# Optimization experiments

Hardware: AMD Instinct MI355X
Metric: run time of the kernel (lower is better)

## Reference

```python
import jax, jax.numpy as jnp
import numpy as np

B, S, SEG, D = 2, 128, 128, 768
RL, H, DK = 16, 8, 64
DV = D // H            # 96, dim_value = dim // heads
NRPF = D // H          # num_rel_pos_features
N = S * RL             # 2048 attention tokens
SCALE = DK ** -0.5


def setup_inputs() -> dict:
    key = jax.random.key(0)
    ks = jax.random.split(key, 12)
    g = lambda k, sh: jax.random.normal(k, sh, jnp.float32) * 0.02
    return {
        'x': jax.random.normal(ks[0], (B, S, SEG, D), jnp.float32),
        'ln_g': jnp.ones((D,), jnp.float32),
        'ln_b': jnp.zeros((D,), jnp.float32),
        'Wq': g(ks[1], (D, H * DK)),
        'Wk': g(ks[2], (D, H * DK)),
        'Wv': g(ks[3], (D, H * DV)),
        'Wr': g(ks[4], (NRPF, H * DK)),
        'r_w_bias': g(ks[5], (H, DK)),
        'r_r_bias': g(ks[6], (H, DK)),
        'Wo': g(ks[7], (H * DV, D)),
        'bo': jnp.zeros((D,), jnp.float32),
        'pos_emb': g(ks[8], (2 * N - 1, NRPF)),  # relative position features, dist -(N-1)..(N-1)
    }


def _layernorm(x, g, b, eps=1e-5):
    mu = jnp.mean(x, -1, keepdims=True)
    var = jnp.var(x, -1, keepdims=True)
    return (x - mu) * jax.lax.rsqrt(var + eps) * g + b


def _relative_shift(t):
    # t: [b, h, n, 2n-1] -> [b, h, n, n] (enformer-style shift)
    b, h, n, _ = t.shape
    t = jnp.pad(t, ((0, 0), (0, 0), (0, 0), (1, 0)))      # [b,h,n,2n]
    t = t.reshape(b, h, 2 * n, n)[:, :, 1:, :]            # [b,h,2n-1,n]
    t = t.reshape(b, h, n, 2 * n - 1)
    return t[..., :n]


def reference(x, ln_g, ln_b, Wq, Wk, Wv, Wr, r_w_bias, r_r_bias, Wo, bo, pos_emb):
    # slice representative tokens per segment and flatten: b s n d -> b (s n) d
    reps = x[:, :, :RL, :].reshape(B, N, D)
    h = _layernorm(reps, ln_g, ln_b)
    q = (h @ Wq).reshape(B, N, H, DK).transpose(0, 2, 1, 3) * SCALE  # bhnd
    k = (h @ Wk).reshape(B, N, H, DK).transpose(0, 2, 1, 3)
    v = (h @ Wv).reshape(B, N, H, DV).transpose(0, 2, 1, 3)
    content = jnp.einsum('bhid,bhjd->bhij', q + r_w_bias[None, :, None, :], k)
    rel_k = (pos_emb @ Wr).reshape(2 * N - 1, H, DK)
    rel = jnp.einsum('bhid,rhd->bhir', q + r_r_bias[None, :, None, :], rel_k)
    logits = content + _relative_shift(rel)
    attn = jax.nn.softmax(logits, axis=-1)
    out = jnp.einsum('bhij,bhjd->bhid', attn, v)
    out = out.transpose(0, 2, 1, 3).reshape(B, N, H * DV) @ Wo + bo
    reps = (reps + out).reshape(B, S, RL, D)  # residual transformer block, un-flatten
    return jnp.concatenate([reps, x[:, :, RL:, :]], axis=2)
```

## Files before the change

### kernel.cpp

```cpp
#include <hip/hip_runtime.h>

typedef short s8v __attribute__((ext_vector_type(8)));
typedef float f4 __attribute__((ext_vector_type(4)));

__device__ inline float bf2f(unsigned short u) {
  union { unsigned i; float f; } x; x.i = (unsigned)u << 16; return x.f;
}
__device__ inline unsigned short f2bf(float f) {
  union { float f; unsigned i; } x; x.f = f;
  return (unsigned short)((x.i + 0x7fffu + ((x.i >> 16) & 1u)) >> 16);
}

__device__ inline void gload16(const void* g, void* l) {
  __builtin_amdgcn_global_load_lds(
      (const __attribute__((address_space(1))) unsigned int*)g,
      (__attribute__((address_space(3))) unsigned int*)l, 16, 0, 0);
}

__global__ __launch_bounds__(256) void copy4(const float4* __restrict__ src,
                                             float4* __restrict__ dst, int n4) {
  int i = blockIdx.x * blockDim.x + threadIdx.x;
  int stride = gridDim.x * blockDim.x;
  for (; i < n4; i += stride) dst[i] = src[i];
}

__global__ __launch_bounds__(256) void ln_kernel(const float* __restrict__ x,
                                                 const float* __restrict__ g,
                                                 const float* __restrict__ bvec,
                                                 unsigned short* __restrict__ h) {
  int m = blockIdx.x;
  int b = m >> 11, n = m & 2047;
  int s = n >> 4, rl = n & 15;
  const float* row = x + ((size_t)((b * 128 + s) * 128 + rl)) * 768;
  int t = threadIdx.x;
  float v0 = row[t], v1 = row[t + 256], v2 = row[t + 512];
  float sum = v0 + v1 + v2;
  float sq = v0 * v0 + v1 * v1 + v2 * v2;
  __shared__ float rs[4], rq[4];
#pragma unroll
  for (int o = 32; o; o >>= 1) {
    sum += __shfl_down(sum, o);
    sq += __shfl_down(sq, o);
  }
  if ((t & 63) == 0) { rs[t >> 6] = sum; rq[t >> 6] = sq; }
  __syncthreads();
  sum = rs[0] + rs[1] + rs[2] + rs[3];
  sq = rq[0] + rq[1] + rq[2] + rq[3];
  float mu = sum * (1.f / 768.f);
  float var = sq * (1.f / 768.f) - mu * mu;
  float inv = rsqrtf(var + 1e-5f);
  unsigned short* hrow = h + (size_t)m * 768;
  hrow[t] = f2bf((v0 - mu) * inv * g[t] + bvec[t]);
  hrow[t + 256] = f2bf((v1 - mu) * inv * g[t + 256] + bvec[t + 256]);
  hrow[t + 512] = f2bf((v2 - mu) * inv * g[t + 512] + bvec[t + 512]);
}

__global__ __launch_bounds__(256) void transp_cvt(const float* __restrict__ Wq,
                                                  const float* __restrict__ Wk,
                                                  const float* __restrict__ Wv,
                                                  const float* __restrict__ Wo,
                                                  unsigned short* __restrict__ Bt,
                                                  unsigned short* __restrict__ Bto) {
  int z = blockIdx.z;
  const float* src; unsigned short* dst; int N;
  if (z == 0) { src = Wq; dst = Bt; N = 512; }
  else if (z == 1) { src = Wk; dst = Bt + (size_t)512 * 768; N = 512; }
  else if (z == 2) { src = Wv; dst = Bt + (size_t)1024 * 768; N = 768; }
  else { src = Wo; dst = Bto; N = 768; }
  int n0 = blockIdx.x << 6, k0 = blockIdx.y << 6;
  if (n0 >= N) return;
  __shared__ float tile[64][65];
  int t = threadIdx.x;
  int c4 = (t & 15) << 2, rr = t >> 4;
#pragma unroll
  for (int i = 0; i < 4; ++i) {
    int kr = rr + (i << 4);
    float4 v = *(const float4*)(src + (size_t)(k0 + kr) * N + n0 + c4);
    tile[c4 + 0][kr] = v.x; tile[c4 + 1][kr] = v.y;
    tile[c4 + 2][kr] = v.z; tile[c4 + 3][kr] = v.w;
  }
  __syncthreads();
  int rowN = t >> 2, kc = (t & 3) << 4;
#pragma unroll
  for (int j = 0; j < 16; ++j)
    dst[(size_t)(n0 + rowN) * 768 + k0 + kc + j] = f2bf(tile[rowN][kc + j]);
}

__global__ __launch_bounds__(256) void gemm_rel(const float* __restrict__ A,
                                                const float* __restrict__ Bw,
                                                unsigned short* __restrict__ C0,
                                                int M, int Nn, int K) {
  __shared__ float As[16][68];
  __shared__ float Bs[16][68];
  int t = threadIdx.x;
  int tx = t & 15, ty = t >> 4;
  int row0 = blockIdx.y << 6, col0 = blockIdx.x << 6;
  float acc[4][4] = {{0.f}};
  int ar = t >> 2, ac = (t & 3) << 2;
  int br = t >> 4, bc = (t & 15) << 2;
  for (int k0 = 0; k0 < K; k0 += 16) {
    float4 av = make_float4(0.f, 0.f, 0.f, 0.f);
    if (row0 + ar < M) av = *(const float4*)(A + (size_t)(row0 + ar) * K + k0 + ac);
    As[ac + 0][ar] = av.x; As[ac + 1][ar] = av.y;
    As[ac + 2][ar] = av.z; As[ac + 3][ar] = av.w;
    float4 bv = *(const float4*)(Bw + (size_t)(k0 + br) * Nn + col0 + bc);
    *(float4*)&Bs[br][bc] = bv;
    __syncthreads();
#pragma unroll
    for (int kk = 0; kk < 16; ++kk) {
      float4 a = *(const float4*)&As[kk][ty << 2];
      float4 b = *(const float4*)&Bs[kk][tx << 2];
      float arr[4] = {a.x, a.y, a.z, a.w};
      float brr[4] = {b.x, b.y, b.z, b.w};
#pragma unroll
      for (int i = 0; i < 4; ++i)
#pragma unroll
        for (int j = 0; j < 4; ++j) acc[i][j] += arr[i] * brr[j];
    }
    __syncthreads();
  }
#pragma unroll
  for (int i = 0; i < 4; ++i) {
    int r = row0 + (ty << 2) + i;
    if (r >= M) continue;
    int colb = col0 + (tx << 2);
    unsigned pk0 = f2bf(acc[i][0]) | ((unsigned)f2bf(acc[i][1]) << 16);
    unsigned pk1 = f2bf(acc[i][2]) | ((unsigned)f2bf(acc[i][3]) << 16);
    *(uint2*)(C0 + (size_t)r * Nn + colb) = make_uint2(pk0, pk1);
  }
}

template <int MODE>
__global__ __launch_bounds__(256) void gemm_mfma(
    const unsigned short* __restrict__ A, const unsigned short* __restrict__ Bt,
    unsigned short* __restrict__ qw, unsigned short* __restrict__ qr,
    unsigned short* __restrict__ kbuf, unsigned short* __restrict__ vt,
    const float* __restrict__ rwb, const float* __restrict__ rrb,
    const float* __restrict__ x, const float* __restrict__ bo,
    float* __restrict__ out) {
  __shared__ __align__(16) short As[128 * 64];
  __shared__ __align__(16) short Bs[128 * 64];
  const int t = threadIdx.x;
  const int w = t >> 6, lane = t & 63;
  const int m16 = lane & 15, quad = lane >> 4;
  const int wm = w >> 1, wn = w & 1;
  const int m0 = blockIdx.y << 7, n0 = blockIdx.x << 7;
  const int K = 768;

  f4 acc[4][4];
#pragma unroll
  for (int i = 0; i < 4; ++i)
#pragma unroll
    for (int j = 0; j < 4; ++j) acc[i][j] = (f4){0.f, 0.f, 0.f, 0.f};

  const int rA = lane >> 3;
  const int cA = lane & 7;

  for (int k0 = 0; k0 < K; k0 += 64) {
    __syncthreads();
#pragma unroll
    for (int i = 0; i < 4; ++i) {
      int seg = (w << 2) + i;
      int r = (seg << 3) + rA;
      int cg = cA ^ (r & 7);
      gload16(A + (size_t)(m0 + r) * K + k0 + (cg << 3), (short*)As + (seg << 9));
      gload16(Bt + (size_t)(n0 + r) * K + k0 + (cg << 3), (short*)Bs + (seg << 9));
    }
    __syncthreads();
#pragma unroll
    for (int kb = 0; kb < 2; ++kb) {
      int cs = ((kb << 2) + quad) ^ (m16 & 7);
      s8v af[4], bf[4];
#pragma unroll
      for (int mt = 0; mt < 4; ++mt) {
        int r = (wm << 6) + (mt << 4) + m16;
        af[mt] = *(const s8v*)(As + (r << 6) + (cs << 3));
      }
#pragma unroll
      for (int nt = 0; nt < 4; ++nt) {
        int rn = (wn << 6) + (nt << 4) + m16;
        bf[nt] = *(const s8v*)(Bs + (rn << 6) + (cs << 3));
      }
#pragma unroll
      for (int mt = 0; mt < 4; ++mt)
#pragma unroll
        for (int nt = 0; nt < 4; ++nt)
          acc[mt][nt] = __builtin_amdgcn_mfma_f32_16x16x32_bf16(af[mt], bf[nt], acc[mt][nt], 0, 0, 0);
    }
  }

#pragma unroll
  for (int nt = 0; nt < 4; ++nt) {
    int n = n0 + (wn << 6) + (nt << 4) + m16;
#pragma unroll
    for (int mt = 0; mt < 4; ++mt) {
#pragma unroll
      for (int rr = 0; rr < 4; ++rr) {
        int m = m0 + (wm << 6) + (mt << 4) + (quad << 2) + rr;
        float v = acc[mt][nt][rr];
        if (MODE == 0) {
          if (n < 512) {
            float vs = v * 0.125f;
            qw[(size_t)m * 512 + n] = f2bf(vs + rwb[n]);
            qr[(size_t)m * 512 + n] = f2bf(vs + rrb[n]);
          } else if (n < 1024) {
            kbuf[(size_t)m * 512 + (n - 512)] = f2bf(v);
          } else {
            int col = n - 1024;
            int b = m >> 11, j = m & 2047;
            vt[(((size_t)(b * 768 + col)) << 11) + j] = f2bf(v);
          }
        } else {
          int b = m >> 11, nn2 = m & 2047;
          int s = nn2 >> 4, rl = nn2 & 15;
          size_t base = ((size_t)((b * 128 + s) * 128 + rl)) * 768;
          out[base + n] = x[base + n] + v + bo[n];
        }
      }
    }
  }
}

__global__ __launch_bounds__(256) void attn_kernel(
    const unsigned short* __restrict__ qw_g, const unsigned short* __restrict__ qr_g,
    const unsigned short* __restrict__ k_g, const unsigned short* __restrict__ vt_g,
    const unsigned short* __restrict__ rk_g, unsigned short* __restrict__ ao) {
  const int qt = blockIdx.x, hh = blockIdx.y, b = blockIdx.z;
  const int i0 = qt << 5;
  const int t = threadIdx.x;
  const int lane = t & 63, w = t >> 6;
  const int m16 = lane & 15, quad = lane >> 4;
  const int mi = w & 1, njb = w >> 1;
  const int sr = t >> 3, sg = t & 7;

  __shared__ __align__(16) short qw_s[32 * 64];
  __shared__ __align__(16) short qr_s[32 * 64];
  __shared__ __align__(16) short k_s[2][64 * 64];
  __shared__ __align__(16) short rk_s[2][96 * 64];
  __shared__ __align__(16) short pb_s[32 * 64];
  __shared__ float p_s[32][68];
  __shared__ short t_s[32][104];
  __shared__ float alpha_s[32];
  __shared__ float linv_s[32];

  for (int u = t; u < 512; u += 256) {
    int tile = u >> 8, idx = u & 255, r = idx >> 3, ch = idx & 7;
    const unsigned short* src =
        (tile ? qr_g : qw_g) + (((size_t)(b * 2048 + i0 + r)) << 9) + (hh << 6) + (ch << 3);
    int4 vdat = *(const int4*)src;
    short* dst = (tile ? qr_s : qw_s) + r * 64 + (((ch ^ (r & 7))) << 3);
    *(int4*)dst = vdat;
  }

  {
    const int rb0 = 2016 - i0;
#pragma unroll
    for (int s = 0; s < 2; ++s) {
      int slot = w * 2 + s;
      int u = (slot << 6) + lane;
      int r = u >> 3, c = u & 7;
      int cg = c ^ (r & 7);
      gload16(k_g + (((size_t)(b * 2048 + r)) << 9) + (hh << 6) + (cg << 3),
              (short*)k_s[0] + (slot << 9));
    }
#pragma unroll
    for (int s = 0; s < 3; ++s) {
      int slot = w * 3 + s;
      int u = (slot << 6) + lane;
      int r = u >> 3, c = u & 7;
      int cg = c ^ (r & 7);
      int grow = rb0 + r; if (grow > 4094) grow = 4094;
      gload16(rk_g + (((size_t)grow) << 9) + (hh << 6) + (cg << 3),
              (short*)rk_s[0] + (slot << 9));
    }
  }
  __syncthreads();

  float m_i = -1e30f, l_i = 0.f;
  f4 o0 = {0.f, 0.f, 0.f, 0.f}, o1 = o0, o2 = o0;
  const int arow = mi * 16 + m16;
  const int asw = arow & 7;
  const int crow = mi * 16 + quad * 4;
  const int brow0 = njb * 16 + m16;
  const int bsw = brow0 & 7;

  const unsigned short* vbase = vt_g + (((size_t)(b * 768 + hh * 96 + brow0)) << 11);

  for (int j0 = 0; j0 < 2048; j0 += 64) {
    const int cur = (j0 >> 6) & 1;

    const unsigned short* vb = vbase + j0;
    s8v va0 = *(const s8v*)(vb + (quad << 3));
    s8v va1 = *(const s8v*)(vb + 65536 + (quad << 3));
    s8v va2 = *(const s8v*)(vb + 131072 + (quad << 3));
    s8v vc0 = *(const s8v*)(vb + ((4 + quad) << 3));
    s8v vc1 = *(const s8v*)(vb + 65536 + ((4 + quad) << 3));
    s8v vc2 = *(const s8v*)(vb + 131072 + ((4 + quad) << 3));

    if (j0 < 1984) {
      const int j0n = j0 + 64;
      const int rbn = 2016 + j0n - i0;
#pragma unroll
      for (int s = 0; s < 2; ++s) {
        int slot = w * 2 + s;
        int u = (slot << 6) + lane;
        int r = u >> 3, c = u & 7;
        int cg = c ^ (r & 7);
        gload16(k_g + (((size_t)(b * 2048 + j0n + r)) << 9) + (hh << 6) + (cg << 3),
                (short*)k_s[cur ^ 1] + (slot << 9));
      }
#pragma unroll
      for (int s = 0; s < 3; ++s) {
        int slot = w * 3 + s;
        int u = (slot << 6) + lane;
        int r = u >> 3, c = u & 7;
        int cg = c ^ (r & 7);
        int grow = rbn + r; if (grow > 4094) grow = 4094;
        gload16(rk_g + (((size_t)grow) << 9) + (hh << 6) + (cg << 3),
                (short*)rk_s[cur ^ 1] + (slot << 9));
      }
    }

    const short* ks = k_s[cur];
    const short* rs = rk_s[cur];
    f4 c0 = {0.f, 0.f, 0.f, 0.f}, c1 = c0;
    f4 r0 = c0, r1 = c0, r2 = c0;
#pragma unroll
    for (int kb = 0; kb < 2; ++kb) {
      const int cidx = (kb << 2) + quad;
      const int co = (cidx ^ asw) << 3;
      const int cb = (cidx ^ bsw) << 3;
      s8v aq = *(const s8v*)(qw_s + arow * 64 + co);
      s8v ar = *(const s8v*)(qr_s + arow * 64 + co);
      s8v bk0 = *(const s8v*)(ks + brow0 * 64 + cb);
      s8v bk1 = *(const s8v*)(ks + (brow0 + 32) * 64 + cb);
      s8v br0 = *(const s8v*)(rs + brow0 * 64 + cb);
      s8v br1 = *(const s8v*)(rs + (brow0 + 32) * 64 + cb);
      s8v br2 = *(const s8v*)(rs + (brow0 + 64) * 64 + cb);
      __builtin_amdgcn_s_setprio(1);
      c0 = __builtin_amdgcn_mfma_f32_16x16x32_bf16(aq, bk0, c0, 0, 0, 0);
      c1 = __builtin_amdgcn_mfma_f32_16x16x32_bf16(aq, bk1, c1, 0, 0, 0);
      r0 = __builtin_amdgcn_mfma_f32_16x16x32_bf16(ar, br0, r0, 0, 0, 0);
      r1 = __builtin_amdgcn_mfma_f32_16x16x32_bf16(ar, br1, r1, 0, 0, 0);
      r2 = __builtin_amdgcn_mfma_f32_16x16x32_bf16(ar, br2, r2, 0, 0, 0);
      __builtin_amdgcn_s_setprio(0);
    }
#pragma unroll
    for (int rr = 0; rr < 4; ++rr) {
      p_s[crow + rr][njb * 16 + m16] = c0[rr];
      p_s[crow + rr][(njb + 2) * 16 + m16] = c1[rr];
      t_s[crow + rr][njb * 16 + m16] = (short)f2bf(r0[rr]);
      t_s[crow + rr][(njb + 2) * 16 + m16] = (short)f2bf(r1[rr]);
      t_s[crow + rr][(njb + 4) * 16 + m16] = (short)f2bf(r2[rr]);
    }
    __syncthreads();

    float sv[8];
    float mx = -1e30f;
#pragma unroll
    for (int j2 = 0; j2 < 8; ++j2) {
      int c = sg + (j2 << 3);
      float s = p_s[sr][c] + bf2f((unsigned short)t_s[sr][c - sr + 31]);
      sv[j2] = s;
      mx = fmaxf(mx, s);
    }
    mx = fmaxf(mx, __shfl_xor(mx, 1));
    mx = fmaxf(mx, __shfl_xor(mx, 2));
    mx = fmaxf(mx, __shfl_xor(mx, 4));
    float m_new = fmaxf(m_i, mx);
    float al = __expf(m_i - m_new);
    float sm = 0.f;
#pragma unroll
    for (int j2 = 0; j2 < 8; ++j2) {
      float p = __expf(sv[j2] - m_new);
      sm += p;
      pb_s[sr * 64 + ((j2 ^ (sr & 7)) << 3) + sg] = (short)f2bf(p);
    }
    sm += __shfl_xor(sm, 1);
    sm += __shfl_xor(sm, 2);
    sm += __shfl_xor(sm, 4);
    l_i = l_i * al + sm;
    m_i = m_new;
    if (sg == 0) alpha_s[sr] = al;
    __syncthreads();

#pragma unroll
    for (int rr = 0; rr < 4; ++rr) {
      float a = alpha_s[crow + rr];
      o0[rr] *= a; o1[rr] *= a; o2[rr] *= a;
    }
#pragma unroll
    for (int kb = 0; kb < 2; ++kb) {
      const int cidx = (kb << 2) + quad;
      const int co = (cidx ^ asw) << 3;
      s8v ap = *(const s8v*)(pb_s + arow * 64 + co);
      s8v b0v = kb ? vc0 : va0;
      s8v b1v = kb ? vc1 : va1;
      s8v b2v = kb ? vc2 : va2;
      __builtin_amdgcn_s_setprio(1);
      o0 = __builtin_amdgcn_mfma_f32_16x16x32_bf16(ap, b0v, o0, 0, 0, 0);
      o1 = __builtin_amdgcn_mfma_f32_16x16x32_bf16(ap, b1v, o1, 0, 0, 0);
      o2 = __builtin_amdgcn_mfma_f32_16x16x32_bf16(ap, b2v, o2, 0, 0, 0);
      __builtin_amdgcn_s_setprio(0);
    }
  }

  if (sg == 0) linv_s[sr] = 1.f / l_i;
  __syncthreads();
#pragma unroll
  for (int rr = 0; rr < 4; ++rr) {
    int row = crow + rr;
    float inv = linv_s[row];
    size_t gbase = ((size_t)(b * 2048 + i0 + row)) * 768 + hh * 96;
    ao[gbase + njb * 16 + m16] = f2bf(o0[rr] * inv);
    ao[gbase + (njb + 2) * 16 + m16] = f2bf(o1[rr] * inv);
    ao[gbase + (njb + 4) * 16 + m16] = f2bf(o2[rr] * inv);
  }
}

extern "C" void kernel_launch(void* const* d_in, const int* in_sizes, int n_in,
                              void* d_out, int out_size, void* d_ws, size_t ws_size,
                              hipStream_t stream) {
  (void)in_sizes; (void)n_in; (void)out_size; (void)ws_size;
  const float* x = (const float*)d_in[0];
  const float* ln_g = (const float*)d_in[1];
  const float* ln_b = (const float*)d_in[2];
  const float* Wq = (const float*)d_in[3];
  const float* Wk = (const float*)d_in[4];
  const float* Wv = (const float*)d_in[5];
  const float* Wr = (const float*)d_in[6];
  const float* rwb = (const float*)d_in[7];
  const float* rrb = (const float*)d_in[8];
  const float* Wo = (const float*)d_in[9];
  const float* bo = (const float*)d_in[10];
  const float* pe = (const float*)d_in[11];
  float* out = (float*)d_out;

  char* p = (char*)d_ws;
  unsigned short* hbf = (unsigned short*)p; p += (size_t)4096 * 768 * 2;
  unsigned short* qw = (unsigned short*)p;  p += (size_t)4096 * 512 * 2;
  unsigned short* qr = (unsigned short*)p;  p += (size_t)4096 * 512 * 2;
  unsigned short* kb = (unsigned short*)p;  p += (size_t)4096 * 512 * 2;
  unsigned short* vt = (unsigned short*)p;  p += (size_t)4096 * 768 * 2;
  unsigned short* rk = (unsigned short*)p;  p += (size_t)4095 * 512 * 2;
  unsigned short* ao = (unsigned short*)p;  p += (size_t)4096 * 768 * 2;
  unsigned short* Bt = (unsigned short*)p;  p += (size_t)1792 * 768 * 2;
  unsigned short* Bto = (unsigned short*)p;

  transp_cvt<<<dim3(12, 12, 4), dim3(256), 0, stream>>>(Wq, Wk, Wv, Wo, Bt, Bto);
  copy4<<<dim3(2048), dim3(256), 0, stream>>>((const float4*)x, (float4*)out, 6291456);
  ln_kernel<<<dim3(4096), dim3(256), 0, stream>>>(x, ln_g, ln_b, hbf);
  gemm_rel<<<dim3(8, 64), dim3(256), 0, stream>>>(pe, Wr, rk, 4095, 512, 96);
  gemm_mfma<0><<<dim3(14, 32), dim3(256), 0, stream>>>(hbf, Bt, qw, qr, kb, vt, rwb, rrb,
                                                       nullptr, nullptr, nullptr);
  attn_kernel<<<dim3(64, 8, 2), dim3(256), 0, stream>>>(qw, qr, kb, vt, rk, ao);
  gemm_mfma<1><<<dim3(6, 32), dim3(256), 0, stream>>>(ao, Bto, nullptr, nullptr, nullptr,
                                                      nullptr, nullptr, nullptr, x, bo, out);
}
```

Baseline: 405.1 us.

## Software-pipeline QK/relative-position MFMAs one tile ahead of softmax and PV

```diff
diff --git a/kernel.cpp b/kernel.cpp
--- a/kernel.cpp
+++ b/kernel.cpp
@@ -239,7 +239,7 @@
   __shared__ __align__(16) short rk_s[2][96 * 64];
   __shared__ __align__(16) short pb_s[32 * 64];
   __shared__ float p_s[32][68];
-  __shared__ short t_s[32][104];
+  __shared__ float t2_s[32][68];
   __shared__ float alpha_s[32];
   __shared__ float linv_s[32];
 
@@ -286,45 +286,12 @@
 
   const unsigned short* vbase = vt_g + (((size_t)(b * 768 + hh * 96 + brow0)) << 11);
 
-  for (int j0 = 0; j0 < 2048; j0 += 64) {
-    const int cur = (j0 >> 6) & 1;
-
-    const unsigned short* vb = vbase + j0;
-    s8v va0 = *(const s8v*)(vb + (quad << 3));
-    s8v va1 = *(const s8v*)(vb + 65536 + (quad << 3));
-    s8v va2 = *(const s8v*)(vb + 131072 + (quad << 3));
-    s8v vc0 = *(const s8v*)(vb + ((4 + quad) << 3));
-    s8v vc1 = *(const s8v*)(vb + 65536 + ((4 + quad) << 3));
-    s8v vc2 = *(const s8v*)(vb + 131072 + ((4 + quad) << 3));
-
-    if (j0 < 1984) {
-      const int j0n = j0 + 64;
-      const int rbn = 2016 + j0n - i0;
-#pragma unroll
-      for (int s = 0; s < 2; ++s) {
-        int slot = w * 2 + s;
-        int u = (slot << 6) + lane;
-        int r = u >> 3, c = u & 7;
-        int cg = c ^ (r & 7);
-        gload16(k_g + (((size_t)(b * 2048 + j0n + r)) << 9) + (hh << 6) + (cg << 3),
-                (short*)k_s[cur ^ 1] + (slot << 9));
-      }
-#pragma unroll
-      for (int s = 0; s < 3; ++s) {
-        int slot = w * 3 + s;
-        int u = (slot << 6) + lane;
-        int r = u >> 3, c = u & 7;
-        int cg = c ^ (r & 7);
-        int grow = rbn + r; if (grow > 4094) grow = 4094;
-        gload16(rk_g + (((size_t)grow) << 9) + (hh << 6) + (cg << 3),
-                (short*)rk_s[cur ^ 1] + (slot << 9));
-      }
-    }
-
-    const short* ks = k_s[cur];
-    const short* rs = rk_s[cur];
-    f4 c0 = {0.f, 0.f, 0.f, 0.f}, c1 = c0;
-    f4 r0 = c0, r1 = c0, r2 = c0;
+  f4 nc0, nc1, nr0, nr1, nr2;
+
+  {
+    const short* ks = k_s[0];
+    const short* rs = rk_s[0];
+    nc0 = (f4){0.f, 0.f, 0.f, 0.f}; nc1 = nc0; nr0 = nc0; nr1 = nc0; nr2 = nc0;
 #pragma unroll
     for (int kb = 0; kb < 2; ++kb) {
       const int cidx = (kb << 2) + quad;
@@ -338,32 +305,120 @@
       s8v br1 = *(const s8v*)(rs + (brow0 + 32) * 64 + cb);
       s8v br2 = *(const s8v*)(rs + (brow0 + 64) * 64 + cb);
       __builtin_amdgcn_s_setprio(1);
-      c0 = __builtin_amdgcn_mfma_f32_16x16x32_bf16(aq, bk0, c0, 0, 0, 0);
-      c1 = __builtin_amdgcn_mfma_f32_16x16x32_bf16(aq, bk1, c1, 0, 0, 0);
-      r0 = __builtin_amdgcn_mfma_f32_16x16x32_bf16(ar, br0, r0, 0, 0, 0);
-      r1 = __builtin_amdgcn_mfma_f32_16x16x32_bf16(ar, br1, r1, 0, 0, 0);
-      r2 = __builtin_amdgcn_mfma_f32_16x16x32_bf16(ar, br2, r2, 0, 0, 0);
+      nc0 = __builtin_amdgcn_mfma_f32_16x16x32_bf16(aq, bk0, nc0, 0, 0, 0);
+      nc1 = __builtin_amdgcn_mfma_f32_16x16x32_bf16(aq, bk1, nc1, 0, 0, 0);
+      nr0 = __builtin_amdgcn_mfma_f32_16x16x32_bf16(ar, br0, nr0, 0, 0, 0);
+      nr1 = __builtin_amdgcn_mfma_f32_16x16x32_bf16(ar, br1, nr1, 0, 0, 0);
+      nr2 = __builtin_amdgcn_mfma_f32_16x16x32_bf16(ar, br2, nr2, 0, 0, 0);
       __builtin_amdgcn_s_setprio(0);
     }
-#pragma unroll
-    for (int rr = 0; rr < 4; ++rr) {
-      p_s[crow + rr][njb * 16 + m16] = c0[rr];
-      p_s[crow + rr][(njb + 2) * 16 + m16] = c1[rr];
-      t_s[crow + rr][njb * 16 + m16] = (short)f2bf(r0[rr]);
-      t_s[crow + rr][(njb + 2) * 16 + m16] = (short)f2bf(r1[rr]);
-      t_s[crow + rr][(njb + 4) * 16 + m16] = (short)f2bf(r2[rr]);
-    }
+  }
+  {
+    const int rbn = 2016 + 64 - i0;
+#pragma unroll
+    for (int s = 0; s < 2; ++s) {
+      int slot = w * 2 + s;
+      int u = (slot << 6) + lane;
+      int r = u >> 3, c = u & 7;
+      int cg = c ^ (r & 7);
+      gload16(k_g + (((size_t)(b * 2048 + 64 + r)) << 9) + (hh << 6) + (cg << 3),
+              (short*)k_s[1] + (slot << 9));
+    }
+#pragma unroll
+    for (int s = 0; s < 3; ++s) {
+      int slot = w * 3 + s;
+      int u = (slot << 6) + lane;
+      int r = u >> 3, c = u & 7;
+      int cg = c ^ (r & 7);
+      int grow = rbn + r; if (grow > 4094) grow = 4094;
+      gload16(rk_g + (((size_t)grow) << 9) + (hh << 6) + (cg << 3),
+              (short*)rk_s[1] + (slot << 9));
+    }
+  }
+#pragma unroll
+  for (int rr = 0; rr < 4; ++rr) {
+    int row = crow + rr;
+    p_s[row][brow0] = nc0[rr];
+    p_s[row][brow0 + 32] = nc1[rr];
+    int cc0 = brow0 + row - 31;
+    t2_s[row][cc0 + 32] = nr1[rr];
+    int csel = cc0 >= 0 ? cc0 : cc0 + 64;
+    float vsel = cc0 >= 0 ? nr0[rr] : nr2[rr];
+    t2_s[row][csel] = vsel;
+  }
+
+  for (int j0 = 0; j0 < 2048; j0 += 64) {
+    const int cur = (j0 >> 6) & 1;
     __syncthreads();
 
+    if (j0 + 128 < 2048) {
+      const int j0p = j0 + 128;
+      const int rbp = 2016 + j0p - i0;
+#pragma unroll
+      for (int s = 0; s < 2; ++s) {
+        int slot = w * 2 + s;
+        int u = (slot << 6) + lane;
+        int r = u >> 3, c = u & 7;
+        int cg = c ^ (r & 7);
+        gload16(k_g + (((size_t)(b * 2048 + j0p + r)) << 9) + (hh << 6) + (cg << 3),
+                (short*)k_s[cur] + (slot << 9));
+      }
+#pragma unroll
+      for (int s = 0; s < 3; ++s) {
+        int slot = w * 3 + s;
+        int u = (slot << 6) + lane;
+        int r = u >> 3, c = u & 7;
+        int cg = c ^ (r & 7);
+        int grow = rbp + r; if (grow > 4094) grow = 4094;
+        gload16(rk_g + (((size_t)grow) << 9) + (hh << 6) + (cg << 3),
+                (short*)rk_s[cur] + (slot << 9));
+      }
+    }
+
+    const bool have_next = (j0 + 64 < 2048);
+    if (have_next) {
+      const short* ks = k_s[cur ^ 1];
+      const short* rs = rk_s[cur ^ 1];
+      nc0 = (f4){0.f, 0.f, 0.f, 0.f}; nc1 = nc0; nr0 = nc0; nr1 = nc0; nr2 = nc0;
+#pragma unroll
+      for (int kb = 0; kb < 2; ++kb) {
+        const int cidx = (kb << 2) + quad;
+        const int co = (cidx ^ asw) << 3;
+        const int cb = (cidx ^ bsw) << 3;
+        s8v aq = *(const s8v*)(qw_s + arow * 64 + co);
+        s8v ar = *(const s8v*)(qr_s + arow * 64 + co);
+        s8v bk0 = *(const s8v*)(ks + brow0 * 64 + cb);
+        s8v bk1 = *(const s8v*)(ks + (brow0 + 32) * 64 + cb);
+        s8v br0 = *(const s8v*)(rs + brow0 * 64 + cb);
+        s8v br1 = *(const s8v*)(rs + (brow0 + 32) * 64 + cb);
+        s8v br2 = *(const s8v*)(rs + (brow0 + 64) * 64 + cb);
+        __builtin_amdgcn_s_setprio(1);
+        nc0 = __builtin_amdgcn_mfma_f32_16x16x32_bf16(aq, bk0, nc0, 0, 0, 0);
+        nc1 = __builtin_amdgcn_mfma_f32_16x16x32_bf16(aq, bk1, nc1, 0, 0, 0);
+        nr0 = __builtin_amdgcn_mfma_f32_16x16x32_bf16(ar, br0, nr0, 0, 0, 0);
+        nr1 = __builtin_amdgcn_mfma_f32_16x16x32_bf16(ar, br1, nr1, 0, 0, 0);
+        nr2 = __builtin_amdgcn_mfma_f32_16x16x32_bf16(ar, br2, nr2, 0, 0, 0);
+        __builtin_amdgcn_s_setprio(0);
+      }
+    }
+
+    const unsigned short* vb = vbase + j0;
+    s8v va0 = *(const s8v*)(vb + (quad << 3));
+    s8v va1 = *(const s8v*)(vb + 65536 + (quad << 3));
+    s8v va2 = *(const s8v*)(vb + 131072 + (quad << 3));
+    s8v vc0 = *(const s8v*)(vb + ((4 + quad) << 3));
+    s8v vc1 = *(const s8v*)(vb + 65536 + ((4 + quad) << 3));
+    s8v vc2 = *(const s8v*)(vb + 131072 + ((4 + quad) << 3));
+
     float sv[8];
-    float mx = -1e30f;
 #pragma unroll
     for (int j2 = 0; j2 < 8; ++j2) {
       int c = sg + (j2 << 3);
-      float s = p_s[sr][c] + bf2f((unsigned short)t_s[sr][c - sr + 31]);
-      sv[j2] = s;
-      mx = fmaxf(mx, s);
-    }
+      sv[j2] = p_s[sr][c] + t2_s[sr][c];
+    }
+    float mxa = fmaxf(fmaxf(sv[0], sv[1]), fmaxf(sv[2], sv[3]));
+    float mxb = fmaxf(fmaxf(sv[4], sv[5]), fmaxf(sv[6], sv[7]));
+    float mx = fmaxf(mxa, mxb);
     mx = fmaxf(mx, __shfl_xor(mx, 1));
     mx = fmaxf(mx, __shfl_xor(mx, 2));
     mx = fmaxf(mx, __shfl_xor(mx, 4));
@@ -402,6 +457,20 @@
       o1 = __builtin_amdgcn_mfma_f32_16x16x32_bf16(ap, b1v, o1, 0, 0, 0);
       o2 = __builtin_amdgcn_mfma_f32_16x16x32_bf16(ap, b2v, o2, 0, 0, 0);
       __builtin_amdgcn_s_setprio(0);
+    }
+
+    if (have_next) {
+#pragma unroll
+      for (int rr = 0; rr < 4; ++rr) {
+        int row = crow + rr;
+        p_s[row][brow0] = nc0[rr];
+        p_s[row][brow0 + 32] = nc1[rr];
+        int cc0 = brow0 + row - 31;
+        t2_s[row][cc0 + 32] = nr1[rr];
+        int csel = cc0 >= 0 ? cc0 : cc0 + 64;
+        float vsel = cc0 >= 0 ? nr0[rr] : nr2[rr];
+        t2_s[row][csel] = vsel;
+      }
     }
   }
 
```

Result: slower. 423.0 us (+4.4%).
